# Optimization experiments

Hardware: AMD Instinct MI355X
Metric: run time of the kernel (lower is better)

The kernel has to match this reference:

```python
import jax, jax.numpy as jnp
import numpy as np
from jax import lax

N_FFT = 16
HOP = 4
WIN_LEN = 16
OUT_WINDOW = 128  # adaptive pool output size
B, L, C = 32, 4096, 64
OUT_FEATURE = 512


def _stft_mag(x_bcl):
    # x_bcl: [B, C, L] float32. Replicates torch.stft(center=True, reflect pad,
    # periodic hann window, onesided) followed by abs().
    win = 0.5 * (1.0 - jnp.cos(2.0 * jnp.pi * jnp.arange(WIN_LEN) / WIN_LEN))  # periodic hann
    pad = N_FFT // 2
    xp = jnp.pad(x_bcl, ((0, 0), (0, 0), (pad, pad)), mode='reflect')
    T = 1 + x_bcl.shape[-1] // HOP  # centered frame count
    idx = np.arange(T)[:, None] * HOP + np.arange(N_FFT)[None, :]  # [T, n_fft] static
    frames = xp[..., idx]                       # [B, C, T, n_fft]
    spec = jnp.fft.rfft(frames * win, axis=-1)  # [B, C, T, F], F = n_fft//2+1
    return jnp.abs(spec).transpose(0, 1, 3, 2)  # [B, C, F, T]


def _adaptive_avg_pool1d(x_nct, out_size):
    # Matches torch adaptive_avg_pool1d: bin i covers [floor(i*N/out), ceil((i+1)*N/out))
    N = x_nct.shape[-1]
    starts = (np.arange(out_size) * N) // out_size
    ends = -((-(np.arange(out_size) + 1) * N) // out_size)  # ceil div
    csum = jnp.concatenate(
        [jnp.zeros(x_nct.shape[:-1] + (1,), x_nct.dtype), jnp.cumsum(x_nct, axis=-1)], axis=-1)
    sums = csum[..., ends] - csum[..., starts]
    counts = jnp.asarray(ends - starts, x_nct.dtype)
    return sums / counts


def setup_inputs() -> dict:
    key = jax.random.key(0)
    k1, k2, k3 = jax.random.split(key, 3)
    in_ch = C * (N_FFT // 2 + 1)  # 576
    x = jax.random.normal(k1, (B, L, C), dtype=jnp.float32)
    fan_in = in_ch * 3
    bound = 1.0 / np.sqrt(fan_in)
    weight = jax.random.uniform(k2, (OUT_FEATURE, in_ch, 3), jnp.float32, -bound, bound)
    bias = jax.random.uniform(k3, (OUT_FEATURE,), jnp.float32, -bound, bound)
    return {"x": x, "weight": weight, "bias": bias}


def reference(x, weight, bias):
    # x: [B, L, C]
    mags = _stft_mag(x.transpose(0, 2, 1))            # [B, C, F, T]
    Bb, Cc, F, T = mags.shape
    m = mags.reshape(Bb, Cc * F, T)                    # [B, C*F, T]
    y = lax.conv_general_dilated(
        m, weight, window_strides=(1,), padding='VALID',
        dimension_numbers=('NCH', 'OIH', 'NCH'))       # [B, out_feature, T-2]
    y = y + bias[None, :, None]
    y = _adaptive_avg_pool1d(y, OUT_WINDOW)            # [B, out_feature, window]
    return y.transpose(0, 2, 1)                        # [B, window, out_feature]
```

## Files before the change

### kernel.cpp

```cpp
#include <hip/hip_runtime.h>
#include <hip/hip_bf16.h>

#define BATCH 32
#define LTOT 4096
#define CCH 64
#define NFFT 16
#define HOP 4
#define NF 9
#define T_FR 1025
#define T_ROWS 1032
#define ICH 576
#define OCH 512
#define TY 1023
#define OUTW 128
#define KTOT 1728

typedef __attribute__((ext_vector_type(8))) _Float16 half8;
typedef __attribute__((ext_vector_type(4))) float floatx4;

__device__ constexpr float C16[16] = {
    1.0f,  0.923879533f,  0.707106781f,  0.382683432f,  0.0f, -0.382683432f,
   -0.707106781f, -0.923879533f, -1.0f, -0.923879533f, -0.707106781f,
   -0.382683432f,  0.0f,  0.382683432f,  0.707106781f,  0.923879533f};
__device__ constexpr float S16[16] = {
    0.0f,  0.382683432f,  0.707106781f,  0.923879533f,  1.0f,  0.923879533f,
    0.707106781f,  0.382683432f,  0.0f, -0.382683432f, -0.707106781f,
   -0.923879533f, -1.0f, -0.923879533f, -0.707106781f, -0.382683432f};

__device__ __forceinline__ void async_copy16(const _Float16* g, _Float16* l) {
  __builtin_amdgcn_global_load_lds(
      (const __attribute__((address_space(1))) unsigned int*)g,
      (__attribute__((address_space(3))) unsigned int*)l, 16, 0, 0);
}

__global__ __launch_bounds__(256) void stft_wrepack_kernel(
    const float* __restrict__ x, const float* __restrict__ weight,
    _Float16* __restrict__ m_ws, _Float16* __restrict__ wkr) {
  const int b = blockIdx.y;
  const int t0 = blockIdx.x * 4;
  const int tid = threadIdx.x;

  const int gid = (b * 258 + blockIdx.x) * 256 + tid;
  if (gid < OCH * ICH) {
    int o = gid / ICH, i = gid - o * ICH;
    int c = i / 9, f = i - c * 9;
    const float* src = weight + (size_t)o * (ICH * 3) + i * 3;
    _Float16* dst = wkr + (size_t)o * KTOT + f * 64 + c;
#pragma unroll
    for (int k = 0; k < 3; ++k)
      dst[k * ICH] = (_Float16)src[k];
  }

  __shared__ float xs[28 * 64];
  const int l0 = t0 * HOP - 8;
  const float* xb = x + (size_t)b * LTOT * CCH;
#pragma unroll
  for (int it = 0; it < 2; ++it) {
    int e = it * 256 + tid;
    int r = e >> 4, c4 = e & 15;
    if (r < 28) {
      int l = l0 + r;
      if (l < 0) l = -l;
      if (l >= LTOT) l = 2 * LTOT - 2 - l;
      *(floatx4*)(&xs[r * 64 + c4 * 4]) =
          *(const floatx4*)(&xb[(size_t)l * CCH + c4 * 4]);
    }
  }
  __syncthreads();

  const int c = tid & 63, tq = tid >> 6;
  const int t = t0 + tq;
  _Float16* o_ptr = m_ws + ((size_t)b * T_ROWS + t) * ICH + c;
  if (t >= T_FR) {
#pragma unroll
    for (int f = 0; f < NF; ++f) o_ptr[f * 64] = (_Float16)0.0f;
    return;
  }
  float wx[16];
#pragma unroll
  for (int j = 0; j < 16; ++j)
    wx[j] = xs[(tq * 4 + j) * 64 + c] * (0.5f * (1.0f - C16[j]));
  float s[8], d[8];
#pragma unroll
  for (int j = 1; j < 8; ++j) {
    s[j] = wx[j] + wx[16 - j];
    d[j] = wx[j] - wx[16 - j];
  }
#pragma unroll
  for (int f = 0; f < NF; ++f) {
    float re = wx[0] + ((f & 1) ? -wx[8] : wx[8]);
    float im = 0.0f;
#pragma unroll
    for (int j = 1; j < 8; ++j) {
      re += s[j] * C16[(f * j) & 15];
      im += d[j] * S16[(f * j) & 15];
    }
    o_ptr[f * 64] = (_Float16)sqrtf(re * re + im * im);
  }
}

__global__ __launch_bounds__(256) void pmean_kernel(
    const _Float16* __restrict__ m_ws, _Float16* __restrict__ pm) {
  const int w = blockIdx.x, b = blockIdx.y;
  const int j = threadIdx.x;
  if (j >= 216) return;
  const int k = j / 72;
  const int i8 = (j - k * 72) * 8;
  const int s = (w * TY) >> 7;
  const int e = ((w + 1) * TY + 127) >> 7;
  const int cnt = e - s;
  const float inv = 1.0f / (float)cnt;
  const _Float16* src =
      m_ws + ((size_t)b * T_ROWS + s + k) * ICH + i8;
  float acc[8];
#pragma unroll
  for (int q = 0; q < 8; ++q) acc[q] = 0.0f;
  for (int t = 0; t < cnt; ++t) {
    half8 v = *(const half8*)(src + (size_t)t * ICH);
#pragma unroll
    for (int q = 0; q < 8; ++q) acc[q] += (float)v[q];
  }
  half8 r;
#pragma unroll
  for (int q = 0; q < 8; ++q) r[q] = (_Float16)(acc[q] * inv);
  *(half8*)(pm + ((size_t)(b * OUTW + w)) * KTOT + j * 8) = r;
}

__global__ __launch_bounds__(256, 2) void gemm_pooled_kernel(
    const _Float16* __restrict__ pm, const _Float16* __restrict__ wkr,
    const float* __restrict__ bias, float* __restrict__ out) {
  const int lid = blockIdx.x;
  const int xcd = lid & 7;
  const int rest = lid >> 3;
  const int m8 = rest & 7;
  const int bq = rest >> 3;
  const int b = bq * 8 + xcd;
  const int o0 = m8 * 64;

  const int tid = threadIdx.x;
  const int wave = tid >> 6, lane = tid & 63;
  const int wm = wave >> 1, wn = wave & 1;

  __shared__ _Float16 as[64 * 64];
  __shared__ _Float16 bs[128 * 64];

  floatx4 acc[2][4];
#pragma unroll
  for (int mt = 0; mt < 2; ++mt)
#pragma unroll
    for (int nt = 0; nt < 4; ++nt)
      acc[mt][nt] = (floatx4)0.0f;

  const int frow = lane & 15;
  const int quad = lane >> 4;
  const int l7 = lane & 7;
  const int srow = lane >> 3;
  const int ssrc_off = srow * KTOT + (l7 ^ srow) * 8;

  const _Float16* ab = wkr + (size_t)o0 * KTOT;
  const _Float16* bb = pm + (size_t)b * OUTW * KTOT;

  for (int kb = 0; kb < 27; ++kb) {
    const int i0 = kb * 64;
#pragma unroll
    for (int it = 0; it < 2; ++it) {
      const int seg = wave * 2 + it;
      async_copy16(ab + (size_t)(seg * 8) * KTOT + i0 + ssrc_off,
                   &as[seg * 512]);
    }
#pragma unroll
    for (int it = 0; it < 4; ++it) {
      const int seg = wave * 4 + it;
      async_copy16(bb + (size_t)(seg * 8) * KTOT + i0 + ssrc_off,
                   &bs[seg * 512]);
    }
    __syncthreads();

#pragma unroll
    for (int kk2 = 0; kk2 < 2; ++kk2) {
      const int jj = kk2 * 4 + quad;
      const int coff = ((jj ^ l7) << 3);
      half8 af[2], bf[4];
#pragma unroll
      for (int mt = 0; mt < 2; ++mt)
        af[mt] = *(const half8*)(&as[(wm * 32 + mt * 16 + frow) * 64 + coff]);
#pragma unroll
      for (int nt = 0; nt < 4; ++nt)
        bf[nt] = *(const half8*)(&bs[(wn * 64 + nt * 16 + frow) * 64 + coff]);
#pragma unroll
      for (int mt = 0; mt < 2; ++mt)
#pragma unroll
        for (int nt = 0; nt < 4; ++nt)
          acc[mt][nt] = __builtin_amdgcn_mfma_f32_16x16x32_f16(
              bf[nt], af[mt], acc[mt][nt], 0, 0, 0);
    }
    __syncthreads();
  }

  const int col = lane & 15;
  float* ob = out + (size_t)b * OUTW * OCH;
#pragma unroll
  for (int nt = 0; nt < 4; ++nt) {
    const int wb = wn * 64 + nt * 16 + quad * 4;
#pragma unroll
    for (int r = 0; r < 4; ++r) {
      const int w = wb + r;
#pragma unroll
      for (int mt = 0; mt < 2; ++mt) {
        const int o = o0 + wm * 32 + mt * 16 + col;
        ob[(size_t)w * OCH + o] = bias[o] + acc[mt][nt][r];
      }
    }
  }
}

extern "C" void kernel_launch(void* const* d_in, const int* in_sizes, int n_in,
                              void* d_out, int out_size, void* d_ws, size_t ws_size,
                              hipStream_t stream) {
  const float* x = (const float*)d_in[0];
  const float* weight = (const float*)d_in[1];
  const float* bias = (const float*)d_in[2];
  float* out = (float*)d_out;

  char* ws = (char*)d_ws;
  const size_t m_bytes = (size_t)BATCH * T_ROWS * ICH * sizeof(_Float16);
  const size_t w_bytes = (size_t)OCH * KTOT * sizeof(_Float16);
  _Float16* m_ws = (_Float16*)ws;
  _Float16* wkr = (_Float16*)(ws + m_bytes);
  _Float16* pm = (_Float16*)(ws + m_bytes + w_bytes);

  hipLaunchKernelGGL(stft_wrepack_kernel, dim3(258, BATCH), dim3(256), 0,
                     stream, x, weight, m_ws, wkr);
  hipLaunchKernelGGL(pmean_kernel, dim3(OUTW, BATCH), dim3(256), 0, stream,
                     m_ws, pm);
  hipLaunchKernelGGL(gemm_pooled_kernel, dim3(256), dim3(256), 0, stream,
                     pm, wkr, bias, out);
}
```

Before: 127.7 us.

## Fuse STFT magnitude and pooled-window averaging into one kernel

The STFT kernel now runs one block per output pool window and batch. It computes the frame magnitudes for that window's range (plus two halo frames for the three conv taps) and accumulates the per-tap window sums in registers, then reduces them across the four thread groups through shared memory. This removes the full fp16 magnitude intermediate, its global write and read-back, and the separate mean kernel launch. In exchange, some frames at window boundaries are recomputed by neighbouring blocks, and the grid shrinks from 258x32 to 128x32 blocks.

```diff
diff --git a/kernel.cpp b/kernel.cpp
--- a/kernel.cpp
+++ b/kernel.cpp
@@ -8,7 +8,6 @@
 #define HOP 4
 #define NF 9
 #define T_FR 1025
-#define T_ROWS 1032
 #define ICH 576
 #define OCH 512
 #define TY 1023
@@ -33,14 +32,13 @@
       (__attribute__((address_space(3))) unsigned int*)l, 16, 0, 0);
 }
 
-__global__ __launch_bounds__(256) void stft_wrepack_kernel(
+__global__ __launch_bounds__(256) void stft_pool_kernel(
     const float* __restrict__ x, const float* __restrict__ weight,
-    _Float16* __restrict__ m_ws, _Float16* __restrict__ wkr) {
-  const int b = blockIdx.y;
-  const int t0 = blockIdx.x * 4;
+    _Float16* __restrict__ pm, _Float16* __restrict__ wkr) {
+  const int w = blockIdx.x, b = blockIdx.y;
   const int tid = threadIdx.x;
 
-  const int gid = (b * 258 + blockIdx.x) * 256 + tid;
+  const int gid = (b * 128 + w) * 256 + tid;
   if (gid < OCH * ICH) {
     int o = gid / ICH, i = gid - o * ICH;
     int c = i / 9, f = i - c * 9;
@@ -51,15 +49,25 @@
       dst[k * ICH] = (_Float16)src[k];
   }
 
-  __shared__ float xs[28 * 64];
-  const int l0 = t0 * HOP - 8;
+  const int s = (w * TY) >> 7;
+  const int e = ((w + 1) * TY + 127) >> 7;
+  const int cnt = e - s;
+  const int R = cnt + 2;
+  const float inv = 1.0f / (float)cnt;
+
+  __shared__ float arena[4 * 27 * 64];
+  float* xs = arena;
+  float* red = arena;
+
+  const int l_base = s * 4 - 8;
+  const int nrow = R * 4 + 12;
   const float* xb = x + (size_t)b * LTOT * CCH;
 #pragma unroll
-  for (int it = 0; it < 2; ++it) {
-    int e = it * 256 + tid;
-    int r = e >> 4, c4 = e & 15;
-    if (r < 28) {
-      int l = l0 + r;
+  for (int it = 0; it < 4; ++it) {
+    int u = it * 256 + tid;
+    int r = u >> 4, c4 = u & 15;
+    if (r < nrow) {
+      int l = l_base + r;
       if (l < 0) l = -l;
       if (l >= LTOT) l = 2 * LTOT - 2 - l;
       *(floatx4*)(&xs[r * 64 + c4 * 4]) =
@@ -69,61 +77,64 @@
   __syncthreads();
 
   const int c = tid & 63, tq = tid >> 6;
-  const int t = t0 + tq;
-  _Float16* o_ptr = m_ws + ((size_t)b * T_ROWS + t) * ICH + c;
-  if (t >= T_FR) {
-#pragma unroll
-    for (int f = 0; f < NF; ++f) o_ptr[f * 64] = (_Float16)0.0f;
-    return;
-  }
-  float wx[16];
-#pragma unroll
-  for (int j = 0; j < 16; ++j)
-    wx[j] = xs[(tq * 4 + j) * 64 + c] * (0.5f * (1.0f - C16[j]));
-  float s[8], d[8];
-#pragma unroll
-  for (int j = 1; j < 8; ++j) {
-    s[j] = wx[j] + wx[16 - j];
-    d[j] = wx[j] - wx[16 - j];
-  }
-#pragma unroll
-  for (int f = 0; f < NF; ++f) {
-    float re = wx[0] + ((f & 1) ? -wx[8] : wx[8]);
-    float im = 0.0f;
-#pragma unroll
-    for (int j = 1; j < 8; ++j) {
-      re += s[j] * C16[(f * j) & 15];
-      im += d[j] * S16[(f * j) & 15];
-    }
-    o_ptr[f * 64] = (_Float16)sqrtf(re * re + im * im);
-  }
-}
-
-__global__ __launch_bounds__(256) void pmean_kernel(
-    const _Float16* __restrict__ m_ws, _Float16* __restrict__ pm) {
-  const int w = blockIdx.x, b = blockIdx.y;
-  const int j = threadIdx.x;
-  if (j >= 216) return;
-  const int k = j / 72;
-  const int i8 = (j - k * 72) * 8;
-  const int s = (w * TY) >> 7;
-  const int e = ((w + 1) * TY + 127) >> 7;
-  const int cnt = e - s;
-  const float inv = 1.0f / (float)cnt;
-  const _Float16* src =
-      m_ws + ((size_t)b * T_ROWS + s + k) * ICH + i8;
-  float acc[8];
-#pragma unroll
-  for (int q = 0; q < 8; ++q) acc[q] = 0.0f;
-  for (int t = 0; t < cnt; ++t) {
-    half8 v = *(const half8*)(src + (size_t)t * ICH);
-#pragma unroll
-    for (int q = 0; q < 8; ++q) acc[q] += (float)v[q];
-  }
-  half8 r;
-#pragma unroll
-  for (int q = 0; q < 8; ++q) r[q] = (_Float16)(acc[q] * inv);
-  *(half8*)(pm + ((size_t)(b * OUTW + w)) * KTOT + j * 8) = r;
+
+  float acc[3][NF];
+#pragma unroll
+  for (int k = 0; k < 3; ++k)
+#pragma unroll
+    for (int f = 0; f < NF; ++f) acc[k][f] = 0.0f;
+
+#pragma unroll
+  for (int it = 0; it < 3; ++it) {
+    const int rl = tq + it * 4;
+    if (rl < R) {
+      float wx[16];
+#pragma unroll
+      for (int j = 0; j < 16; ++j)
+        wx[j] = xs[(rl * 4 + j) * 64 + c] * (0.5f * (1.0f - C16[j]));
+      float sj[8], dj[8];
+#pragma unroll
+      for (int j = 1; j < 8; ++j) {
+        sj[j] = wx[j] + wx[16 - j];
+        dj[j] = wx[j] - wx[16 - j];
+      }
+#pragma unroll
+      for (int f = 0; f < NF; ++f) {
+        float re = wx[0] + ((f & 1) ? -wx[8] : wx[8]);
+        float im = 0.0f;
+#pragma unroll
+        for (int j = 1; j < 8; ++j) {
+          re += sj[j] * C16[(f * j) & 15];
+          im += dj[j] * S16[(f * j) & 15];
+        }
+        const float mag = (float)(_Float16)sqrtf(re * re + im * im);
+#pragma unroll
+        for (int k = 0; k < 3; ++k)
+          if ((unsigned)(rl - k) < (unsigned)cnt) acc[k][f] += mag;
+      }
+    }
+  }
+
+  __syncthreads();
+
+#pragma unroll
+  for (int k = 0; k < 3; ++k)
+#pragma unroll
+    for (int f = 0; f < NF; ++f)
+      red[((tq * 27) + k * 9 + f) * 64 + c] = acc[k][f];
+  __syncthreads();
+
+  _Float16* pmo = pm + ((size_t)b * OUTW + w) * KTOT;
+  for (int j = tid; j < KTOT; j += 256) {
+    const int k = j / ICH;
+    const int rem = j - k * ICH;
+    const int f = rem >> 6;
+    const int cc = rem & 63;
+    const int base = (k * 9 + f) * 64 + cc;
+    const float sum = red[base] + red[27 * 64 + base] +
+                      red[2 * 27 * 64 + base] + red[3 * 27 * 64 + base];
+    pmo[j] = (_Float16)(sum * inv);
+  }
 }
 
 __global__ __launch_bounds__(256, 2) void gemm_pooled_kernel(
@@ -223,16 +234,12 @@
   float* out = (float*)d_out;
 
   char* ws = (char*)d_ws;
-  const size_t m_bytes = (size_t)BATCH * T_ROWS * ICH * sizeof(_Float16);
   const size_t w_bytes = (size_t)OCH * KTOT * sizeof(_Float16);
-  _Float16* m_ws = (_Float16*)ws;
-  _Float16* wkr = (_Float16*)(ws + m_bytes);
-  _Float16* pm = (_Float16*)(ws + m_bytes + w_bytes);
-
-  hipLaunchKernelGGL(stft_wrepack_kernel, dim3(258, BATCH), dim3(256), 0,
-                     stream, x, weight, m_ws, wkr);
-  hipLaunchKernelGGL(pmean_kernel, dim3(OUTW, BATCH), dim3(256), 0, stream,
-                     m_ws, pm);
+  _Float16* wkr = (_Float16*)ws;
+  _Float16* pm = (_Float16*)(ws + w_bytes);
+
+  hipLaunchKernelGGL(stft_pool_kernel, dim3(OUTW, BATCH), dim3(256), 0,
+                     stream, x, weight, pm, wkr);
   hipLaunchKernelGGL(gemm_pooled_kernel, dim3(256), dim3(256), 0, stream,
                      pm, wkr, bias, out);
 }
```

Result: slower. 132.1 us (+3.5%).
